# Optimization experiments

Measured on AMD Instinct MI355X. Metric: run time of the kernel, lower is better.

Reference implementation:

```python
import jax, jax.numpy as jnp
import numpy as np

TEMPERATURE = 0.1  # use_temperature=True


def setup_inputs() -> dict:
    key = jax.random.key(0)
    # encoder output features: [batch_size, num_epoch, feature_dim]
    feature = jax.random.normal(key, (128, 64, 128), dtype=jnp.float32)
    return {"feature": feature}


def reference(feature):
    # L2-normalize along feature dim (F.normalize, p=2, dim=1 on flat features)
    f = feature / jnp.linalg.norm(feature, axis=-1, keepdims=True)
    B, E, D = f.shape
    # full pairwise logits: [B, E, E, B]
    logits = jnp.einsum('ijk,mnk->ijnm', f, f) / TEMPERATURE
    e = jnp.exp(logits)
    idx = jnp.arange(B)
    # mask[i, j, :, i] = 1 -> positives are the m == i block: e[i, j, :, i]
    pos = e[idx, :, :, idx].sum(-1)              # [B, E]
    neg = e.sum(axis=(2, 3)) - pos               # [B, E] everything else
    loss = (-jnp.log(pos / (pos + neg))).mean()
    return loss
```

## Files before the change

### kernel.cpp

```cpp
#include <hip/hip_runtime.h>
#include <hip/hip_bf16.h>

#define N_ROWS 8192
#define DIM    128
#define TILE   128
#define CPG    8
#define EXPTEN 22026.465794806718f
#define SCALE  3.7982826f

typedef __attribute__((ext_vector_type(8))) short short8;
typedef __attribute__((ext_vector_type(4))) float floatx4;

#define EXP2F(x) __builtin_amdgcn_exp2f(x)

#define GLOAD_LDS(g, l)                                                        \
    __builtin_amdgcn_global_load_lds(                                          \
        (const __attribute__((address_space(1))) void*)(g),                    \
        (__attribute__((address_space(3))) void*)(l), 16, 0, 0)

__global__ void norm_kernel(const float* __restrict__ F, __hip_bfloat16* __restrict__ Xb,
                            float* __restrict__ pos, float* __restrict__ den) {
    int lane = threadIdx.x & 63;
    int wave = threadIdx.x >> 6;
    int row  = blockIdx.x * 4 + wave;
    const float2 v = *(const float2*)(F + (size_t)row * DIM + lane * 2);
    float ss = v.x * v.x + v.y * v.y;
    #pragma unroll
    for (int m = 1; m < 64; m <<= 1) ss += __shfl_xor(ss, m);
    float inv = rsqrtf(ss) * SCALE;
    __hip_bfloat162 o;
    o.x = __float2bfloat16(v.x * inv);
    o.y = __float2bfloat16(v.y * inv);
    *((__hip_bfloat162*)(Xb + (size_t)row * DIM) + lane) = o;
    if (lane == 0) { pos[row] = 0.f; den[row] = 0.f; }
}

__global__ __launch_bounds__(256, 2) void gram_kernel(
        const __hip_bfloat16* __restrict__ Xb,
        float* __restrict__ pos, float* __restrict__ den) {
    __shared__ __hip_bfloat16 Bs[2][TILE * DIM];
    const int tid  = threadIdx.x;
    const int rb   = blockIdx.x;
    const int cg   = blockIdx.y;
    const int lane = tid & 63;
    const int wave = tid >> 6;
    const int wm   = wave >> 1, wn = wave & 1;
    const int quad = lane >> 4;
    const int l15  = lane & 15;

    short8 af[4][4];
    {
        const __hip_bfloat16* Ab = Xb + ((size_t)(rb * TILE + wm * 64 + l15)) * DIM + quad * 8;
        #pragma unroll
        for (int mi = 0; mi < 4; ++mi)
            #pragma unroll
            for (int ko = 0; ko < 4; ++ko)
                af[mi][ko] = *(const short8*)(Ab + mi * 16 * DIM + ko * 32);
    }

    float dp[4][4];
    #pragma unroll
    for (int a = 0; a < 4; ++a)
        #pragma unroll
        for (int b = 0; b < 4; ++b) dp[a][b] = 0.f;

    auto stage = [&](int ct, int buf) {
        #pragma unroll
        for (int i = 0; i < 8; ++i) {
            int chunk = (i * 4 + wave) * 64 + lane;
            int r  = chunk >> 4;
            int cs = (chunk & 15) ^ (r & 15);
            const __hip_bfloat16* gp = Xb + ((size_t)(ct * TILE + r)) * DIM + cs * 8;
            char* lp = (char*)&Bs[buf][0] + (i * 4 + wave) * 1024;
            GLOAD_LDS(gp, lp);
        }
    };

    auto compute = [&](int ct, int buf) {
        floatx4 acc[4][4];
        #pragma unroll
        for (int mi = 0; mi < 4; ++mi)
            #pragma unroll
            for (int ni = 0; ni < 4; ++ni) acc[mi][ni] = (floatx4)0.0f;

        const char* Bb = (const char*)&Bs[buf][0];
        #pragma unroll
        for (int ko = 0; ko < 4; ++ko) {
            short8 bf[4];
            #pragma unroll
            for (int ni = 0; ni < 4; ++ni) {
                int r  = wn * 64 + ni * 16 + l15;
                int ch = (ko * 4 + quad) ^ l15;
                bf[ni] = *(const short8*)(Bb + r * 256 + ch * 16);
            }
            #pragma unroll
            for (int mi = 0; mi < 4; ++mi)
                #pragma unroll
                for (int ni = 0; ni < 4; ++ni)
                    acc[mi][ni] = __builtin_amdgcn_mfma_f32_16x16x32_bf16(
                        af[mi][ko], bf[ni], acc[mi][ni], 0, 0, 0);
        }

        const bool pos_tile = (ct == rb) && (wm == wn);
        #pragma unroll
        for (int mi = 0; mi < 4; ++mi)
            #pragma unroll
            for (int rg = 0; rg < 4; ++rg) {
                float dadd = 0.f;
                #pragma unroll
                for (int ni = 0; ni < 4; ++ni)
                    dadd += EXP2F(acc[mi][ni][rg]);
                if (pos_tile) {
                    if (l15 == quad * 4 + rg)
                        dadd += EXPTEN - EXP2F(acc[mi][mi][rg]);
                    float p = dadd;
                    #pragma unroll
                    for (int m = 1; m < 16; m <<= 1) p += __shfl_xor(p, m);
                    if (l15 == 0)
                        atomicAdd(&pos[rb * TILE + wm * 64 + mi * 16 + quad * 4 + rg], p);
                }
                dp[mi][rg] += dadd;
            }
    };

    stage(cg * CPG, 0);
    __syncthreads();
    #pragma unroll 1
    for (int t = 0; t < CPG - 1; ++t) {
        stage(cg * CPG + t + 1, (t + 1) & 1);
        compute(cg * CPG + t, t & 1);
        __syncthreads();
    }
    compute(cg * CPG + CPG - 1, (CPG - 1) & 1);

    #pragma unroll
    for (int mi = 0; mi < 4; ++mi)
        #pragma unroll
        for (int rg = 0; rg < 4; ++rg) {
            float d = dp[mi][rg];
            #pragma unroll
            for (int m = 1; m < 16; m <<= 1) d += __shfl_xor(d, m);
            if (l15 == 0)
                atomicAdd(&den[rb * TILE + wm * 64 + mi * 16 + quad * 4 + rg], d);
        }
}

__global__ void loss_kernel(const float* __restrict__ pos, const float* __restrict__ den,
                            float* __restrict__ out) {
    __shared__ float red[4];
    float acc = 0.f;
    for (int i = threadIdx.x; i < N_ROWS / 4; i += 256) {
        float4 d = ((const float4*)den)[i];
        float4 p = ((const float4*)pos)[i];
        acc += __logf(d.x / p.x) + __logf(d.y / p.y) +
               __logf(d.z / p.z) + __logf(d.w / p.w);
    }
    #pragma unroll
    for (int m = 1; m < 64; m <<= 1) acc += __shfl_xor(acc, m);
    int lane = threadIdx.x & 63, w = threadIdx.x >> 6;
    if (lane == 0) red[w] = acc;
    __syncthreads();
    if (threadIdx.x == 0)
        out[0] = (red[0] + red[1] + red[2] + red[3]) * (1.0f / (float)N_ROWS);
}

extern "C" void kernel_launch(void* const* d_in, const int* in_sizes, int n_in,
                              void* d_out, int out_size, void* d_ws, size_t ws_size,
                              hipStream_t stream) {
    const float* feature = (const float*)d_in[0];
    float* pos = (float*)d_ws;
    float* den = pos + N_ROWS;
    __hip_bfloat16* Xb = (__hip_bfloat16*)(den + N_ROWS);

    norm_kernel<<<N_ROWS / 4, 256, 0, stream>>>(feature, Xb, pos, den);
    gram_kernel<<<dim3(64, 8), 256, 0, stream>>>(Xb, pos, den);
    loss_kernel<<<1, 256, 0, stream>>>(pos, den, (float*)d_out);
}
```

Measured before the change: 86.17 us.

## Exploit Gram matrix symmetry by computing only upper-triangular tiles

The kernel now walks only the upper-triangular tile pairs (2080 of 4096) of the symmetric similarity matrix, split across 512 blocks. Each off-diagonal tile adds its exp sums to both the row denominators and, through column reductions, the column denominators. This roughly halves the MFMA and exp work. In exchange it adds column shuffles and extra atomics, a serial tile-index search in each block, and A-fragment reloads whenever a block crosses into a new row.

```diff
diff --git a/kernel.cpp b/kernel.cpp
--- a/kernel.cpp
+++ b/kernel.cpp
@@ -4,7 +4,8 @@
 #define N_ROWS 8192
 #define DIM    128
 #define TILE   128
-#define CPG    8
+#define NTILES 64
+#define NBLK   512
 #define EXPTEN 22026.465794806718f
 #define SCALE  3.7982826f
 
@@ -40,23 +41,29 @@
         float* __restrict__ pos, float* __restrict__ den) {
     __shared__ __hip_bfloat16 Bs[2][TILE * DIM];
     const int tid  = threadIdx.x;
-    const int rb   = blockIdx.x;
-    const int cg   = blockIdx.y;
     const int lane = tid & 63;
     const int wave = tid >> 6;
     const int wm   = wave >> 1, wn = wave & 1;
     const int quad = lane >> 4;
     const int l15  = lane & 15;
 
+    const int blk = blockIdx.x;
+    const int s = (blk * 65) >> 4;
+    const int e = ((blk + 1) * 65) >> 4;
+
+    int rb = 0, off = 0;
+    while (off + (NTILES - rb) <= s) { off += NTILES - rb; ++rb; }
+    int cb = rb + (s - off);
+
     short8 af[4][4];
-    {
-        const __hip_bfloat16* Ab = Xb + ((size_t)(rb * TILE + wm * 64 + l15)) * DIM + quad * 8;
+    auto loadA = [&](int r) {
+        const __hip_bfloat16* Ab = Xb + ((size_t)(r * TILE + wm * 64 + l15)) * DIM + quad * 8;
         #pragma unroll
         for (int mi = 0; mi < 4; ++mi)
             #pragma unroll
             for (int ko = 0; ko < 4; ++ko)
                 af[mi][ko] = *(const short8*)(Ab + mi * 16 * DIM + ko * 32);
-    }
+    };
 
     float dp[4][4];
     #pragma unroll
@@ -76,7 +83,21 @@
         }
     };
 
-    auto compute = [&](int ct, int buf) {
+    auto flush_dp = [&](int r) {
+        #pragma unroll
+        for (int mi = 0; mi < 4; ++mi)
+            #pragma unroll
+            for (int rg = 0; rg < 4; ++rg) {
+                float d = dp[mi][rg];
+                #pragma unroll
+                for (int m = 1; m < 16; m <<= 1) d += __shfl_xor(d, m);
+                if (l15 == 0)
+                    atomicAdd(&den[r * TILE + wm * 64 + mi * 16 + quad * 4 + rg], d);
+                dp[mi][rg] = 0.f;
+            }
+    };
+
+    auto compute = [&](int crb, int ccb, int buf) {
         floatx4 acc[4][4];
         #pragma unroll
         for (int mi = 0; mi < 4; ++mi)
@@ -101,15 +122,22 @@
                         af[mi][ko], bf[ni], acc[mi][ni], 0, 0, 0);
         }
 
-        const bool pos_tile = (ct == rb) && (wm == wn);
+        const bool diag     = (ccb == crb);
+        const bool pos_tile = diag && (wm == wn);
+        float cacc[4] = {0.f, 0.f, 0.f, 0.f};
         #pragma unroll
         for (int mi = 0; mi < 4; ++mi)
             #pragma unroll
             for (int rg = 0; rg < 4; ++rg) {
-                float dadd = 0.f;
-                #pragma unroll
-                for (int ni = 0; ni < 4; ++ni)
-                    dadd += EXP2F(acc[mi][ni][rg]);
+                float ex0 = EXP2F(acc[mi][0][rg]);
+                float ex1 = EXP2F(acc[mi][1][rg]);
+                float ex2 = EXP2F(acc[mi][2][rg]);
+                float ex3 = EXP2F(acc[mi][3][rg]);
+                float dadd = (ex0 + ex1) + (ex2 + ex3);
+                if (!diag) {
+                    cacc[0] += ex0; cacc[1] += ex1;
+                    cacc[2] += ex2; cacc[3] += ex3;
+                }
                 if (pos_tile) {
                     if (l15 == quad * 4 + rg)
                         dadd += EXPTEN - EXP2F(acc[mi][mi][rg]);
@@ -117,32 +145,42 @@
                     #pragma unroll
                     for (int m = 1; m < 16; m <<= 1) p += __shfl_xor(p, m);
                     if (l15 == 0)
-                        atomicAdd(&pos[rb * TILE + wm * 64 + mi * 16 + quad * 4 + rg], p);
+                        atomicAdd(&pos[crb * TILE + wm * 64 + mi * 16 + quad * 4 + rg], p);
                 }
                 dp[mi][rg] += dadd;
             }
-    };
-
-    stage(cg * CPG, 0);
+        if (!diag) {
+            #pragma unroll
+            for (int ni = 0; ni < 4; ++ni) {
+                float c2 = cacc[ni];
+                c2 += __shfl_xor(c2, 16);
+                c2 += __shfl_xor(c2, 32);
+                if (quad == 0)
+                    atomicAdd(&den[ccb * TILE + wn * 64 + ni * 16 + l15], c2);
+            }
+        }
+    };
+
+    loadA(rb);
+    stage(cb, 0);
     __syncthreads();
+    const int nt = e - s;
     #pragma unroll 1
-    for (int t = 0; t < CPG - 1; ++t) {
-        stage(cg * CPG + t + 1, (t + 1) & 1);
-        compute(cg * CPG + t, t & 1);
+    for (int i = 0; i < nt; ++i) {
+        int nrb = rb, ncb = cb + 1;
+        if (ncb == NTILES) { ++nrb; ncb = nrb; }
+        if (i + 1 < nt) stage(ncb, (i + 1) & 1);
+        compute(rb, cb, i & 1);
         __syncthreads();
+        if (i + 1 < nt) {
+            if (nrb != rb) {
+                flush_dp(rb);
+                loadA(nrb);
+            }
+            rb = nrb; cb = ncb;
+        }
     }
-    compute(cg * CPG + CPG - 1, (CPG - 1) & 1);
-
-    #pragma unroll
-    for (int mi = 0; mi < 4; ++mi)
-        #pragma unroll
-        for (int rg = 0; rg < 4; ++rg) {
-            float d = dp[mi][rg];
-            #pragma unroll
-            for (int m = 1; m < 16; m <<= 1) d += __shfl_xor(d, m);
-            if (l15 == 0)
-                atomicAdd(&den[rb * TILE + wm * 64 + mi * 16 + quad * 4 + rg], d);
-        }
+    flush_dp(rb);
 }
 
 __global__ void loss_kernel(const float* __restrict__ pos, const float* __restrict__ den,
@@ -173,6 +211,6 @@
     __hip_bfloat16* Xb = (__hip_bfloat16*)(den + N_ROWS);
 
     norm_kernel<<<N_ROWS / 4, 256, 0, stream>>>(feature, Xb, pos, den);
-    gram_kernel<<<dim3(64, 8), 256, 0, stream>>>(Xb, pos, den);
+    gram_kernel<<<NBLK, 256, 0, stream>>>(Xb, pos, den);
     loss_kernel<<<1, 256, 0, stream>>>(pos, den, (float*)d_out);
 }
```

Result: slower. 95.35 us (+10.7%).

## Load B fragments directly from global into registers, dropping LDS staging

Applied to the files above, without the earlier changes.

Removes the double-buffered LDS staging of column tiles (global_load_lds plus barriers). Each wave now loads its B fragments straight from global memory into registers and computes MFMA per (mi,ni) block with a single accumulator, applying exp right away. This cuts LDS traffic, syncs and accumulator registers, but loses data sharing between waves and the load/compute overlap, so it leans on L2/L1 for reuse.

```diff
diff --git a/kernel.cpp b/kernel.cpp
--- a/kernel.cpp
+++ b/kernel.cpp
@@ -12,11 +12,6 @@
 typedef __attribute__((ext_vector_type(4))) float floatx4;
 
 #define EXP2F(x) __builtin_amdgcn_exp2f(x)
-
-#define GLOAD_LDS(g, l)                                                        \
-    __builtin_amdgcn_global_load_lds(                                          \
-        (const __attribute__((address_space(1))) void*)(g),                    \
-        (__attribute__((address_space(3))) void*)(l), 16, 0, 0)
 
 __global__ void norm_kernel(const float* __restrict__ F, __hip_bfloat16* __restrict__ Xb,
                             float* __restrict__ pos, float* __restrict__ den) {
@@ -38,7 +33,6 @@
 __global__ __launch_bounds__(256, 2) void gram_kernel(
         const __hip_bfloat16* __restrict__ Xb,
         float* __restrict__ pos, float* __restrict__ den) {
-    __shared__ __hip_bfloat16 Bs[2][TILE * DIM];
     const int tid  = threadIdx.x;
     const int rb   = blockIdx.x;
     const int cg   = blockIdx.y;
@@ -64,74 +58,49 @@
         #pragma unroll
         for (int b = 0; b < 4; ++b) dp[a][b] = 0.f;
 
-    auto stage = [&](int ct, int buf) {
+    #pragma unroll 1
+    for (int t = 0; t < CPG; ++t) {
+        const int ct = cg * CPG + t;
+        const __hip_bfloat16* Bb = Xb + ((size_t)(ct * TILE + wn * 64 + l15)) * DIM + quad * 8;
+        short8 bf[4][4];
         #pragma unroll
-        for (int i = 0; i < 8; ++i) {
-            int chunk = (i * 4 + wave) * 64 + lane;
-            int r  = chunk >> 4;
-            int cs = (chunk & 15) ^ (r & 15);
-            const __hip_bfloat16* gp = Xb + ((size_t)(ct * TILE + r)) * DIM + cs * 8;
-            char* lp = (char*)&Bs[buf][0] + (i * 4 + wave) * 1024;
-            GLOAD_LDS(gp, lp);
-        }
-    };
-
-    auto compute = [&](int ct, int buf) {
-        floatx4 acc[4][4];
-        #pragma unroll
-        for (int mi = 0; mi < 4; ++mi)
+        for (int ni = 0; ni < 4; ++ni)
             #pragma unroll
-            for (int ni = 0; ni < 4; ++ni) acc[mi][ni] = (floatx4)0.0f;
-
-        const char* Bb = (const char*)&Bs[buf][0];
-        #pragma unroll
-        for (int ko = 0; ko < 4; ++ko) {
-            short8 bf[4];
-            #pragma unroll
-            for (int ni = 0; ni < 4; ++ni) {
-                int r  = wn * 64 + ni * 16 + l15;
-                int ch = (ko * 4 + quad) ^ l15;
-                bf[ni] = *(const short8*)(Bb + r * 256 + ch * 16);
-            }
-            #pragma unroll
-            for (int mi = 0; mi < 4; ++mi)
-                #pragma unroll
-                for (int ni = 0; ni < 4; ++ni)
-                    acc[mi][ni] = __builtin_amdgcn_mfma_f32_16x16x32_bf16(
-                        af[mi][ko], bf[ni], acc[mi][ni], 0, 0, 0);
-        }
+            for (int ko = 0; ko < 4; ++ko)
+                bf[ni][ko] = *(const short8*)(Bb + ni * 16 * DIM + ko * 32);
 
         const bool pos_tile = (ct == rb) && (wm == wn);
         #pragma unroll
-        for (int mi = 0; mi < 4; ++mi)
+        for (int mi = 0; mi < 4; ++mi) {
+            float dadd[4] = {0.f, 0.f, 0.f, 0.f};
+            #pragma unroll
+            for (int ni = 0; ni < 4; ++ni) {
+                floatx4 acc = (floatx4)0.0f;
+                #pragma unroll
+                for (int ko = 0; ko < 4; ++ko)
+                    acc = __builtin_amdgcn_mfma_f32_16x16x32_bf16(
+                        af[mi][ko], bf[ni][ko], acc, 0, 0, 0);
+                #pragma unroll
+                for (int rg = 0; rg < 4; ++rg) {
+                    float ex = EXP2F(acc[rg]);
+                    if (pos_tile && ni == mi && l15 == quad * 4 + rg)
+                        ex = EXPTEN;
+                    dadd[rg] += ex;
+                }
+            }
             #pragma unroll
             for (int rg = 0; rg < 4; ++rg) {
-                float dadd = 0.f;
-                #pragma unroll
-                for (int ni = 0; ni < 4; ++ni)
-                    dadd += EXP2F(acc[mi][ni][rg]);
                 if (pos_tile) {
-                    if (l15 == quad * 4 + rg)
-                        dadd += EXPTEN - EXP2F(acc[mi][mi][rg]);
-                    float p = dadd;
+                    float p = dadd[rg];
                     #pragma unroll
                     for (int m = 1; m < 16; m <<= 1) p += __shfl_xor(p, m);
                     if (l15 == 0)
                         atomicAdd(&pos[rb * TILE + wm * 64 + mi * 16 + quad * 4 + rg], p);
                 }
-                dp[mi][rg] += dadd;
+                dp[mi][rg] += dadd[rg];
             }
-    };
-
-    stage(cg * CPG, 0);
-    __syncthreads();
-    #pragma unroll 1
-    for (int t = 0; t < CPG - 1; ++t) {
-        stage(cg * CPG + t + 1, (t + 1) & 1);
-        compute(cg * CPG + t, t & 1);
-        __syncthreads();
+        }
     }
-    compute(cg * CPG + CPG - 1, (CPG - 1) & 1);
 
     #pragma unroll
     for (int mi = 0; mi < 4; ++mi)
```

Result: slower. 101.9 us (+18.3%).

## Pipeline gram kernel with four-slot 64-column LDS ring and explicit vmcnt waits

Applied to the files above, without the earlier changes.

Replaces the two-buffer 128-column tile loop with a four-slot ring of 64-column half tiles, prefetched three ahead and gated by explicit s_waitcnt vmcnt counts and raw barriers instead of __syncthreads. Each wave now covers 64x32 of output per step. B fragments are preloaded from LDS before the MFMA loop, which is wrapped in s_setprio. The positive-block handling is restructured so that only the diagonal half tile takes the extra branch. This aims to hide global-to-LDS latency and cut barrier stalls, at the risk of depending on hand-counted vmcnt values and accepting smaller per-step work with more barriers.

```diff
diff --git a/kernel.cpp b/kernel.cpp
--- a/kernel.cpp
+++ b/kernel.cpp
@@ -4,7 +4,7 @@
 #define N_ROWS 8192
 #define DIM    128
 #define TILE   128
-#define CPG    8
+#define NHALF  16
 #define EXPTEN 22026.465794806718f
 #define SCALE  3.7982826f
 
@@ -12,6 +12,8 @@
 typedef __attribute__((ext_vector_type(4))) float floatx4;
 
 #define EXP2F(x) __builtin_amdgcn_exp2f(x)
+#define BAR()    __builtin_amdgcn_s_barrier()
+#define VMCNT(n) asm volatile("s_waitcnt vmcnt(" #n ")" ::: "memory")
 
 #define GLOAD_LDS(g, l)                                                        \
     __builtin_amdgcn_global_load_lds(                                          \
@@ -38,7 +40,7 @@
 __global__ __launch_bounds__(256, 2) void gram_kernel(
         const __hip_bfloat16* __restrict__ Xb,
         float* __restrict__ pos, float* __restrict__ den) {
-    __shared__ __hip_bfloat16 Bs[2][TILE * DIM];
+    __shared__ __hip_bfloat16 Bs[4][64 * DIM];
     const int tid  = threadIdx.x;
     const int rb   = blockIdx.x;
     const int cg   = blockIdx.y;
@@ -48,15 +50,30 @@
     const int quad = lane >> 4;
     const int l15  = lane & 15;
 
+    auto stage = [&](int h) {
+        char* slot = (char*)&Bs[h & 3][0];
+        const int colbase = cg * (NHALF * 64) + h * 64;
+        #pragma unroll
+        for (int i = 0; i < 4; ++i) {
+            int chunk = (i * 4 + wave) * 64 + lane;
+            int r  = chunk >> 4;
+            int cs = (chunk & 15) ^ (r & 15);
+            const __hip_bfloat16* gp = Xb + ((size_t)(colbase + r)) * DIM + cs * 8;
+            GLOAD_LDS(gp, slot + (i * 4 + wave) * 1024);
+        }
+    };
+
     short8 af[4][4];
     {
-        const __hip_bfloat16* Ab = Xb + ((size_t)(rb * TILE + wm * 64 + l15)) * DIM + quad * 8;
+        const __hip_bfloat16* Ab =
+            Xb + ((size_t)(rb * TILE + wm * 64 + l15)) * DIM + quad * 8;
         #pragma unroll
         for (int mi = 0; mi < 4; ++mi)
             #pragma unroll
             for (int ko = 0; ko < 4; ++ko)
                 af[mi][ko] = *(const short8*)(Ab + mi * 16 * DIM + ko * 32);
     }
+    stage(0); stage(1); stage(2);
 
     float dp[4][4];
     #pragma unroll
@@ -64,74 +81,87 @@
         #pragma unroll
         for (int b = 0; b < 4; ++b) dp[a][b] = 0.f;
 
-    auto stage = [&](int ct, int buf) {
-        #pragma unroll
-        for (int i = 0; i < 8; ++i) {
-            int chunk = (i * 4 + wave) * 64 + lane;
-            int r  = chunk >> 4;
-            int cs = (chunk & 15) ^ (r & 15);
-            const __hip_bfloat16* gp = Xb + ((size_t)(ct * TILE + r)) * DIM + cs * 8;
-            char* lp = (char*)&Bs[buf][0] + (i * 4 + wave) * 1024;
-            GLOAD_LDS(gp, lp);
-        }
-    };
-
-    auto compute = [&](int ct, int buf) {
-        floatx4 acc[4][4];
+    auto compute = [&](int h) {
+        const char* Bb = (const char*)&Bs[h & 3][0];
+        const bool pos_half = (cg * NHALF + h) == (rb * 2 + wm);
+
+        short8 bf[2][4];
+        #pragma unroll
+        for (int ni = 0; ni < 2; ++ni)
+            #pragma unroll
+            for (int ko = 0; ko < 4; ++ko) {
+                int r  = wn * 32 + ni * 16 + l15;
+                int ch = (ko * 4 + quad) ^ l15;
+                bf[ni][ko] = *(const short8*)(Bb + r * 256 + ch * 16);
+            }
+
+        floatx4 acc[4][2];
         #pragma unroll
         for (int mi = 0; mi < 4; ++mi)
             #pragma unroll
-            for (int ni = 0; ni < 4; ++ni) acc[mi][ni] = (floatx4)0.0f;
-
-        const char* Bb = (const char*)&Bs[buf][0];
-        #pragma unroll
-        for (int ko = 0; ko < 4; ++ko) {
-            short8 bf[4];
-            #pragma unroll
-            for (int ni = 0; ni < 4; ++ni) {
-                int r  = wn * 64 + ni * 16 + l15;
-                int ch = (ko * 4 + quad) ^ l15;
-                bf[ni] = *(const short8*)(Bb + r * 256 + ch * 16);
-            }
-            #pragma unroll
-            for (int mi = 0; mi < 4; ++mi)
-                #pragma unroll
-                for (int ni = 0; ni < 4; ++ni)
+            for (int ni = 0; ni < 2; ++ni) acc[mi][ni] = (floatx4)0.0f;
+
+        __builtin_amdgcn_s_setprio(1);
+        #pragma unroll
+        for (int ko = 0; ko < 4; ++ko)
+            #pragma unroll
+            for (int mi = 0; mi < 4; ++mi)
+                #pragma unroll
+                for (int ni = 0; ni < 2; ++ni)
                     acc[mi][ni] = __builtin_amdgcn_mfma_f32_16x16x32_bf16(
-                        af[mi][ko], bf[ni], acc[mi][ni], 0, 0, 0);
-        }
-
-        const bool pos_tile = (ct == rb) && (wm == wn);
-        #pragma unroll
-        for (int mi = 0; mi < 4; ++mi)
-            #pragma unroll
-            for (int rg = 0; rg < 4; ++rg) {
-                float dadd = 0.f;
-                #pragma unroll
-                for (int ni = 0; ni < 4; ++ni)
-                    dadd += EXP2F(acc[mi][ni][rg]);
-                if (pos_tile) {
-                    if (l15 == quad * 4 + rg)
-                        dadd += EXPTEN - EXP2F(acc[mi][mi][rg]);
-                    float p = dadd;
+                        af[mi][ko], bf[ni][ko], acc[mi][ni], 0, 0, 0);
+        __builtin_amdgcn_s_setprio(0);
+
+        if (!pos_half) {
+            #pragma unroll
+            for (int mi = 0; mi < 4; ++mi)
+                #pragma unroll
+                for (int ni = 0; ni < 2; ++ni)
+                    #pragma unroll
+                    for (int rg = 0; rg < 4; ++rg)
+                        dp[mi][rg] += EXP2F(acc[mi][ni][rg]);
+        } else {
+            float padd[4][4];
+            #pragma unroll
+            for (int mi = 0; mi < 4; ++mi)
+                #pragma unroll
+                for (int rg = 0; rg < 4; ++rg) padd[mi][rg] = 0.f;
+            #pragma unroll
+            for (int mi = 0; mi < 4; ++mi)
+                #pragma unroll
+                for (int ni = 0; ni < 2; ++ni)
+                    #pragma unroll
+                    for (int rg = 0; rg < 4; ++rg) {
+                        float ex = EXP2F(acc[mi][ni][rg]);
+                        if (mi == wn * 2 + ni && l15 == quad * 4 + rg)
+                            ex = EXPTEN;
+                        dp[mi][rg]   += ex;
+                        padd[mi][rg] += ex;
+                    }
+            #pragma unroll
+            for (int mi = 0; mi < 4; ++mi)
+                #pragma unroll
+                for (int rg = 0; rg < 4; ++rg) {
+                    float p = padd[mi][rg];
                     #pragma unroll
                     for (int m = 1; m < 16; m <<= 1) p += __shfl_xor(p, m);
                     if (l15 == 0)
                         atomicAdd(&pos[rb * TILE + wm * 64 + mi * 16 + quad * 4 + rg], p);
                 }
-                dp[mi][rg] += dadd;
-            }
+        }
     };
 
-    stage(cg * CPG, 0);
-    __syncthreads();
     #pragma unroll 1
-    for (int t = 0; t < CPG - 1; ++t) {
-        stage(cg * CPG + t + 1, (t + 1) & 1);
-        compute(cg * CPG + t, t & 1);
-        __syncthreads();
+    for (int h = 0; h < NHALF - 3; ++h) {
+        BAR();
+        stage(h + 3);
+        VMCNT(12);
+        BAR();
+        compute(h);
     }
-    compute(cg * CPG + CPG - 1, (CPG - 1) & 1);
+    VMCNT(8);  BAR(); compute(NHALF - 3);
+    VMCNT(4);  BAR(); compute(NHALF - 2);
+    VMCNT(0);  BAR(); compute(NHALF - 1);
 
     #pragma unroll
     for (int mi = 0; mi < 4; ++mi)
```

Result: no change. 86.86 us (+0.8%).
